# Performance work log

Measured on AMD Instinct MI355X. Metric: run time of the kernel, lower is better.

## Reference

```python
import jax, jax.numpy as jnp
import numpy as np

N = 8_000_000   # total nodes across the batch
B = 2048        # number of graphs (segments)
L1 = 1.0 / 50.0


def _bce(p, t):
    # elementwise BCE matching torch.nn.BCELoss: logs clamped at -100
    logp = jnp.clip(jnp.log(p), -100.0)
    log1mp = jnp.clip(jnp.log1p(-p), -100.0)
    return -(t * logp + (1.0 - t) * log1mp)


def setup_inputs() -> dict:
    key = jax.random.key(0)
    k1, k2, k3, k4, k5, k6 = jax.random.split(key, 6)
    y_mus_pred = jax.random.uniform(k1, (N,), dtype=jnp.float32)
    y_mus = jax.random.uniform(k2, (N,), dtype=jnp.float32)
    y_sat_pred = jax.random.uniform(k3, (B,), dtype=jnp.float32)
    y_sat = jax.random.uniform(k4, (B,), dtype=jnp.float32)
    batch = jnp.sort(jax.random.randint(k5, (N,), 0, B, dtype=jnp.int32))
    mask = jax.random.randint(k6, (N,), 0, 2, dtype=jnp.int32)
    return {"y_mus_pred": y_mus_pred, "y_mus": y_mus,
            "y_sat_pred": y_sat_pred, "y_sat": y_sat,
            "batch": batch, "mask": mask}


def reference(y_mus_pred, y_mus, y_sat_pred, y_sat, batch, mask):
    m = mask.astype(y_mus_pred.dtype)
    # per-node BCE on masked predictions (torch: bce_mus(pred*mask, target), reduction='sum' per graph)
    bce = _bce(y_mus_pred * m, y_mus)                      # [N]
    seg_bce = jax.ops.segment_sum(bce, batch, num_segments=B)  # [B]
    seg_cnt = jax.ops.segment_sum(m, batch, num_segments=B)    # [B] = sum(mask) per graph
    per_graph = jnp.where(seg_cnt > 0, seg_bce / jnp.maximum(seg_cnt, 1.0), 0.0)
    total = per_graph.sum()
    # scalar saturation BCE (mean reduction) scaled by L1
    total = total + _bce(y_sat_pred, y_sat).mean() * jnp.asarray(L1, y_sat_pred.dtype)
    return total
```

## Files before the change

kernel.cpp:

```cpp
#include <hip/hip_runtime.h>

#define BLOCK 256

__device__ __forceinline__ float bce_elem(float p, float t) {
    float lp  = fmaxf(__logf(p), -100.0f);
    float l1p = fmaxf(__logf(1.0f - p), -100.0f);
    return -__builtin_fmaf(t, lp - l1p, l1p);
}

__device__ __forceinline__ int lower_bound(const int* __restrict__ a, int n, int v) {
    int lo = 0, hi = n;
    while (lo < hi) {
        int mid = (int)(((unsigned)lo + (unsigned)hi) >> 1);
        if (a[mid] < v) lo = mid + 1; else hi = mid;
    }
    return lo;
}

__global__ __launch_bounds__(BLOCK) void seg_kernel(
    const float* __restrict__ pred, const float* __restrict__ tgt,
    const int* __restrict__ batch, const int* __restrict__ mask,
    const float* __restrict__ sat_pred, const float* __restrict__ sat_tgt,
    float* __restrict__ per_graph, int n, int Bseg)
{
    const int b   = blockIdx.x;
    const int tid = threadIdx.x;

    __shared__ int sh_lo, sh_hi;
    if (tid == 0) sh_lo = lower_bound(batch, n, b);
    if (tid == 1) sh_hi = lower_bound(batch, n, b + 1);
    __syncthreads();
    const int lo = sh_lo, hi = sh_hi;

    float accb = 0.0f, accc = 0.0f;

    int a0 = (lo + 3) & ~3;
    if (a0 > hi) a0 = hi;
    const int nvec = (hi - a0) >> 2;
    const int a1   = a0 + (nvec << 2);

    for (int i = lo + tid; i < a0; i += BLOCK) {
        float mf = (float)mask[i];
        accb += bce_elem(pred[i] * mf, tgt[i]);
        accc += mf;
    }
    const float4* p4 = reinterpret_cast<const float4*>(pred) + (a0 >> 2);
    const float4* t4 = reinterpret_cast<const float4*>(tgt)  + (a0 >> 2);
    const int4*   m4 = reinterpret_cast<const int4*>(mask)   + (a0 >> 2);
    for (int i = tid; i < nvec; i += BLOCK) {
        float4 p = p4[i];
        float4 t = t4[i];
        int4   m = m4[i];
        float m0 = (float)m.x, m1 = (float)m.y, m2 = (float)m.z, m3 = (float)m.w;
        accb += bce_elem(p.x * m0, t.x);  accc += m0;
        accb += bce_elem(p.y * m1, t.y);  accc += m1;
        accb += bce_elem(p.z * m2, t.z);  accc += m2;
        accb += bce_elem(p.w * m3, t.w);  accc += m3;
    }
    for (int i = a1 + tid; i < hi; i += BLOCK) {
        float mf = (float)mask[i];
        accb += bce_elem(pred[i] * mf, tgt[i]);
        accc += mf;
    }

    #pragma unroll
    for (int o = 32; o > 0; o >>= 1) {
        accb += __shfl_xor(accb, o);
        accc += __shfl_xor(accc, o);
    }
    __shared__ float wb[4], wc[4];
    if ((tid & 63) == 0) { wb[tid >> 6] = accb; wc[tid >> 6] = accc; }
    __syncthreads();
    if (tid == 0) {
        float sb = wb[0] + wb[1] + wb[2] + wb[3];
        float sc = wc[0] + wc[1] + wc[2] + wc[3];
        float pg = (sc > 0.0f) ? sb / fmaxf(sc, 1.0f) : 0.0f;
        pg += bce_elem(sat_pred[b], sat_tgt[b]) * ((1.0f / 50.0f) / (float)Bseg);
        per_graph[b] = pg;
    }
}

__global__ __launch_bounds__(256) void sum_kernel(
    const float* __restrict__ per_graph, float* __restrict__ out, int Bseg)
{
    float local = 0.0f;
    for (int i = threadIdx.x; i < Bseg; i += 256) local += per_graph[i];
    #pragma unroll
    for (int o = 32; o > 0; o >>= 1) local += __shfl_xor(local, o);
    __shared__ float ws[4];
    if ((threadIdx.x & 63) == 0) ws[threadIdx.x >> 6] = local;
    __syncthreads();
    if (threadIdx.x == 0) out[0] = ws[0] + ws[1] + ws[2] + ws[3];
}

extern "C" void kernel_launch(void* const* d_in, const int* in_sizes, int n_in,
                              void* d_out, int out_size, void* d_ws, size_t ws_size,
                              hipStream_t stream) {
    const float* y_mus_pred = (const float*)d_in[0];
    const float* y_mus      = (const float*)d_in[1];
    const float* y_sat_pred = (const float*)d_in[2];
    const float* y_sat      = (const float*)d_in[3];
    const int*   batch      = (const int*)d_in[4];
    const int*   mask       = (const int*)d_in[5];

    const int n    = in_sizes[0];
    const int Bseg = in_sizes[2];

    float* per_graph = (float*)d_ws;

    seg_kernel<<<Bseg, BLOCK, 0, stream>>>(
        y_mus_pred, y_mus, batch, mask, y_sat_pred, y_sat, per_graph, n, Bseg);
    sum_kernel<<<1, 256, 0, stream>>>(per_graph, (float*)d_out, Bseg);
}
```

Measured before the change: 154.8 us.

## Use wave-parallel 65-ary segment search and triple-unroll vector loads

Segment boundary search moves from a single-thread binary search to a wave-wide 65-way search using ballot and popcount. This cuts the number of dependent global-memory round trips before the block can start streaming. The main float4 loop is unrolled three-way so more loads are in flight per thread, and launch bounds ask for 8 blocks per CU. The trade-offs are more registers per thread and extra search loads from the wave-parallel probes.

Result: no change. 152.2 us (-1.7%).

```diff
diff --git a/kernel.cpp b/kernel.cpp
--- a/kernel.cpp
+++ b/kernel.cpp
@@ -8,16 +8,37 @@
     return -__builtin_fmaf(t, lp - l1p, l1p);
 }
 
-__device__ __forceinline__ int lower_bound(const int* __restrict__ a, int n, int v) {
+__device__ __forceinline__ int wave_lower_bound(const int* __restrict__ a, int n, int v) {
+    const int lane = threadIdx.x & 63;
     int lo = 0, hi = n;
-    while (lo < hi) {
-        int mid = (int)(((unsigned)lo + (unsigned)hi) >> 1);
-        if (a[mid] < v) lo = mid + 1; else hi = mid;
+    while (hi - lo > 64) {
+        int range  = hi - lo;
+        int stride = range / 65 + 1;
+        int idx    = lo + (lane + 1) * stride;
+        bool lt    = (idx < hi) && (a[idx] < v);
+        int  c     = __popcll(__ballot(lt));
+        int  nlo   = lo + c * stride;
+        int  nhi   = nlo + stride;
+        if (nhi > hi) nhi = hi;
+        lo = nlo; hi = nhi;
     }
-    return lo;
+    int idx = lo + lane;
+    bool ge = (idx >= hi) || (a[idx] >= v);
+    unsigned long long bal = __ballot(ge);
+    return bal ? (lo + __ffsll(bal) - 1) : hi;
 }
 
-__global__ __launch_bounds__(BLOCK) void seg_kernel(
+#define PROC(p, t, m)                                                          \
+    do {                                                                       \
+        float m0 = (float)(m).x, m1 = (float)(m).y,                            \
+              m2 = (float)(m).z, m3 = (float)(m).w;                            \
+        accb += bce_elem((p).x * m0, (t).x);  accc += m0;                      \
+        accb += bce_elem((p).y * m1, (t).y);  accc += m1;                      \
+        accb += bce_elem((p).z * m2, (t).z);  accc += m2;                      \
+        accb += bce_elem((p).w * m3, (t).w);  accc += m3;                      \
+    } while (0)
+
+__global__ __launch_bounds__(BLOCK, 8) void seg_kernel(
     const float* __restrict__ pred, const float* __restrict__ tgt,
     const int* __restrict__ batch, const int* __restrict__ mask,
     const float* __restrict__ sat_pred, const float* __restrict__ sat_tgt,
@@ -26,11 +47,14 @@
     const int b   = blockIdx.x;
     const int tid = threadIdx.x;
 
-    __shared__ int sh_lo, sh_hi;
-    if (tid == 0) sh_lo = lower_bound(batch, n, b);
-    if (tid == 1) sh_hi = lower_bound(batch, n, b + 1);
+    __shared__ int sh_bounds[2];
+    const int wid = tid >> 6;
+    if (wid < 2) {
+        int r = wave_lower_bound(batch, n, b + wid);
+        if ((tid & 63) == 0) sh_bounds[wid] = r;
+    }
     __syncthreads();
-    const int lo = sh_lo, hi = sh_hi;
+    const int lo = sh_bounds[0], hi = sh_bounds[1];
 
     float accb = 0.0f, accc = 0.0f;
 
@@ -44,22 +68,31 @@
         accb += bce_elem(pred[i] * mf, tgt[i]);
         accc += mf;
     }
+
     const float4* p4 = reinterpret_cast<const float4*>(pred) + (a0 >> 2);
     const float4* t4 = reinterpret_cast<const float4*>(tgt)  + (a0 >> 2);
     const int4*   m4 = reinterpret_cast<const int4*>(mask)   + (a0 >> 2);
-    for (int i = tid; i < nvec; i += BLOCK) {
+
+    int i = tid;
+    const int nv2 = nvec - 2 * BLOCK;
+    for (; i < nv2; i += 3 * BLOCK) {
+        float4 pa = p4[i], pb = p4[i + BLOCK], pc = p4[i + 2 * BLOCK];
+        float4 ta = t4[i], tb = t4[i + BLOCK], tc = t4[i + 2 * BLOCK];
+        int4   ma = m4[i], mb = m4[i + BLOCK], mc = m4[i + 2 * BLOCK];
+        PROC(pa, ta, ma);
+        PROC(pb, tb, mb);
+        PROC(pc, tc, mc);
+    }
+    for (; i < nvec; i += BLOCK) {
         float4 p = p4[i];
         float4 t = t4[i];
         int4   m = m4[i];
-        float m0 = (float)m.x, m1 = (float)m.y, m2 = (float)m.z, m3 = (float)m.w;
-        accb += bce_elem(p.x * m0, t.x);  accc += m0;
-        accb += bce_elem(p.y * m1, t.y);  accc += m1;
-        accb += bce_elem(p.z * m2, t.z);  accc += m2;
-        accb += bce_elem(p.w * m3, t.w);  accc += m3;
+        PROC(p, t, m);
     }
-    for (int i = a1 + tid; i < hi; i += BLOCK) {
-        float mf = (float)mask[i];
-        accb += bce_elem(pred[i] * mf, tgt[i]);
+
+    for (int j = a1 + tid; j < hi; j += BLOCK) {
+        float mf = (float)mask[j];
+        accb += bce_elem(pred[j] * mf, tgt[j]);
         accc += mf;
     }
 
```

## Replace per-segment blocks with grid-stride streaming and wave-reduced atomics

Applied to the files above, without the earlier changes.

Replaces the one-block-per-graph kernel, which binary-searched segment bounds, with a grid-stride streaming kernel that also reads the sorted batch ids. Each wave reduces its partial sums and issues atomics per segment, with a fallback for segment boundaries, and a finalize kernel does the division and saturation term. This is meant to fix the load imbalance and low memory-level parallelism of the segment-per-block design. The cost is reading an extra array, a memset, and float atomics that make summation order nondeterministic.

After: 222.9 us. 43.9% more time.

```diff
diff --git a/kernel.cpp b/kernel.cpp
--- a/kernel.cpp
+++ b/kernel.cpp
@@ -1,6 +1,10 @@
 #include <hip/hip_runtime.h>
 
 #define BLOCK 256
+#define NB    2048
+
+typedef float fx4 __attribute__((ext_vector_type(4)));
+typedef int   ix4 __attribute__((ext_vector_type(4)));
 
 __device__ __forceinline__ float bce_elem(float p, float t) {
     float lp  = fmaxf(__logf(p), -100.0f);
@@ -8,83 +12,83 @@
     return -__builtin_fmaf(t, lp - l1p, l1p);
 }
 
-__device__ __forceinline__ int lower_bound(const int* __restrict__ a, int n, int v) {
-    int lo = 0, hi = n;
-    while (lo < hi) {
-        int mid = (int)(((unsigned)lo + (unsigned)hi) >> 1);
-        if (a[mid] < v) lo = mid + 1; else hi = mid;
-    }
-    return lo;
-}
-
-__global__ __launch_bounds__(BLOCK) void seg_kernel(
+__global__ __launch_bounds__(BLOCK, 8) void stream_kernel(
     const float* __restrict__ pred, const float* __restrict__ tgt,
     const int* __restrict__ batch, const int* __restrict__ mask,
-    const float* __restrict__ sat_pred, const float* __restrict__ sat_tgt,
-    float* __restrict__ per_graph, int n, int Bseg)
+    float* __restrict__ acc_b, float* __restrict__ acc_c, int n)
 {
-    const int b   = blockIdx.x;
-    const int tid = threadIdx.x;
+    const int tid  = blockIdx.x * BLOCK + threadIdx.x;
+    const int lane = threadIdx.x & 63;
+    const int ngroups  = n >> 2;
+    const int nthreads = NB * BLOCK;
 
-    __shared__ int sh_lo, sh_hi;
-    if (tid == 0) sh_lo = lower_bound(batch, n, b);
-    if (tid == 1) sh_hi = lower_bound(batch, n, b + 1);
-    __syncthreads();
-    const int lo = sh_lo, hi = sh_hi;
+    const fx4* p4 = reinterpret_cast<const fx4*>(pred);
+    const fx4* t4 = reinterpret_cast<const fx4*>(tgt);
+    const ix4* m4 = reinterpret_cast<const ix4*>(mask);
+    const ix4* b4 = reinterpret_cast<const ix4*>(batch);
 
-    float accb = 0.0f, accc = 0.0f;
+    for (int g = tid; g < ngroups; g += nthreads) {
+        fx4 p = __builtin_nontemporal_load(p4 + g);
+        fx4 t = __builtin_nontemporal_load(t4 + g);
+        ix4 m = __builtin_nontemporal_load(m4 + g);
+        ix4 s = __builtin_nontemporal_load(b4 + g);
 
-    int a0 = (lo + 3) & ~3;
-    if (a0 > hi) a0 = hi;
-    const int nvec = (hi - a0) >> 2;
-    const int a1   = a0 + (nvec << 2);
+        float m0 = (float)m[0], m1 = (float)m[1],
+              m2 = (float)m[2], m3 = (float)m[3];
+        float v0 = bce_elem(p[0] * m0, t[0]);
+        float v1 = bce_elem(p[1] * m1, t[1]);
+        float v2 = bce_elem(p[2] * m2, t[2]);
+        float v3 = bce_elem(p[3] * m3, t[3]);
+        float vb = (v0 + v1) + (v2 + v3);
+        float vc = (m0 + m1) + (m2 + m3);
 
-    for (int i = lo + tid; i < a0; i += BLOCK) {
-        float mf = (float)mask[i];
-        accb += bce_elem(pred[i] * mf, tgt[i]);
-        accc += mf;
-    }
-    const float4* p4 = reinterpret_cast<const float4*>(pred) + (a0 >> 2);
-    const float4* t4 = reinterpret_cast<const float4*>(tgt)  + (a0 >> 2);
-    const int4*   m4 = reinterpret_cast<const int4*>(mask)   + (a0 >> 2);
-    for (int i = tid; i < nvec; i += BLOCK) {
-        float4 p = p4[i];
-        float4 t = t4[i];
-        int4   m = m4[i];
-        float m0 = (float)m.x, m1 = (float)m.y, m2 = (float)m.z, m3 = (float)m.w;
-        accb += bce_elem(p.x * m0, t.x);  accc += m0;
-        accb += bce_elem(p.y * m1, t.y);  accc += m1;
-        accb += bce_elem(p.z * m2, t.z);  accc += m2;
-        accb += bce_elem(p.w * m3, t.w);  accc += m3;
-    }
-    for (int i = a1 + tid; i < hi; i += BLOCK) {
-        float mf = (float)mask[i];
-        accb += bce_elem(pred[i] * mf, tgt[i]);
-        accc += mf;
+        const int  wave_base = g - lane;
+        const bool wave_full = (wave_base + 63) < ngroups;
+        const int  slo = __shfl(s[0], 0);
+        const int  shi = __shfl(s[3], 63);
+
+        if (wave_full && slo == shi) {
+            #pragma unroll
+            for (int o = 32; o > 0; o >>= 1) {
+                vb += __shfl_xor(vb, o);
+                vc += __shfl_xor(vc, o);
+            }
+            if (lane == 0) {
+                atomicAdd(&acc_b[slo], vb);
+                atomicAdd(&acc_c[slo], vc);
+            }
+        } else if (s[0] == s[3]) {
+            atomicAdd(&acc_b[s[0]], vb);
+            atomicAdd(&acc_c[s[0]], vc);
+        } else {
+            atomicAdd(&acc_b[s[0]], v0);  atomicAdd(&acc_c[s[0]], m0);
+            atomicAdd(&acc_b[s[1]], v1);  atomicAdd(&acc_c[s[1]], m1);
+            atomicAdd(&acc_b[s[2]], v2);  atomicAdd(&acc_c[s[2]], m2);
+            atomicAdd(&acc_b[s[3]], v3);  atomicAdd(&acc_c[s[3]], m3);
+        }
     }
 
-    #pragma unroll
-    for (int o = 32; o > 0; o >>= 1) {
-        accb += __shfl_xor(accb, o);
-        accc += __shfl_xor(accc, o);
-    }
-    __shared__ float wb[4], wc[4];
-    if ((tid & 63) == 0) { wb[tid >> 6] = accb; wc[tid >> 6] = accc; }
-    __syncthreads();
     if (tid == 0) {
-        float sb = wb[0] + wb[1] + wb[2] + wb[3];
-        float sc = wc[0] + wc[1] + wc[2] + wc[3];
-        float pg = (sc > 0.0f) ? sb / fmaxf(sc, 1.0f) : 0.0f;
-        pg += bce_elem(sat_pred[b], sat_tgt[b]) * ((1.0f / 50.0f) / (float)Bseg);
-        per_graph[b] = pg;
+        for (int i = (ngroups << 2); i < n; ++i) {
+            float mf = (float)mask[i];
+            atomicAdd(&acc_b[batch[i]], bce_elem(pred[i] * mf, tgt[i]));
+            atomicAdd(&acc_c[batch[i]], mf);
+        }
     }
 }
 
-__global__ __launch_bounds__(256) void sum_kernel(
-    const float* __restrict__ per_graph, float* __restrict__ out, int Bseg)
+__global__ __launch_bounds__(256) void finalize_kernel(
+    const float* __restrict__ acc_b, const float* __restrict__ acc_c,
+    const float* __restrict__ sat_pred, const float* __restrict__ sat_tgt,
+    float* __restrict__ out, int Bseg)
 {
     float local = 0.0f;
-    for (int i = threadIdx.x; i < Bseg; i += 256) local += per_graph[i];
+    for (int i = threadIdx.x; i < Bseg; i += 256) {
+        float c  = acc_c[i];
+        float pg = (c > 0.0f) ? acc_b[i] / fmaxf(c, 1.0f) : 0.0f;
+        pg += bce_elem(sat_pred[i], sat_tgt[i]) * ((1.0f / 50.0f) / (float)Bseg);
+        local += pg;
+    }
     #pragma unroll
     for (int o = 32; o > 0; o >>= 1) local += __shfl_xor(local, o);
     __shared__ float ws[4];
@@ -106,9 +110,12 @@
     const int n    = in_sizes[0];
     const int Bseg = in_sizes[2];
 
-    float* per_graph = (float*)d_ws;
+    float* acc_b = (float*)d_ws;
+    float* acc_c = acc_b + Bseg;
 
-    seg_kernel<<<Bseg, BLOCK, 0, stream>>>(
-        y_mus_pred, y_mus, batch, mask, y_sat_pred, y_sat, per_graph, n, Bseg);
-    sum_kernel<<<1, 256, 0, stream>>>(per_graph, (float*)d_out, Bseg);
+    hipMemsetAsync(acc_b, 0, 2 * Bseg * sizeof(float), stream);
+    stream_kernel<<<NB, BLOCK, 0, stream>>>(
+        y_mus_pred, y_mus, batch, mask, acc_b, acc_c, n);
+    finalize_kernel<<<1, 256, 0, stream>>>(
+        acc_b, acc_c, y_sat_pred, y_sat, (float*)d_out, Bseg);
 }
```
